# Performance work log

Hardware: AMD Instinct MI355X
Metric: run time of the kernel (lower is better)

Reference implementation:

```python
import jax, jax.numpy as jnp
import numpy as np
from jax import lax

N, S, K, V, C, D, NH, NB, HD = 4, 1024, 4, 32000, 1000, 512, 8, 6, 2048
DH = D // NH
CAP = round((S // K) * 1.0)  # expert capacity = Seq//K * capacity_factor


def setup_inputs() -> dict:
    key = jax.random.key(0)
    ks = jax.random.split(key, 12)
    nrm = lambda k, shape: jax.random.normal(k, shape, dtype=jnp.float32) * 0.02
    return dict(
        x_in=jax.random.randint(ks[0], (N, S), 0, V),
        y_target=jax.random.randint(ks[1], (N, S), 0, C),
        tok_emb=nrm(ks[2], (K, V, D)),
        pos_emb=nrm(ks[3], (K, S, D)),
        ln1_s=jnp.ones((K, NB, D)), ln1_b=jnp.zeros((K, NB, D)),
        Wqkv=nrm(ks[4], (K, NB, D, 3 * D)), bqkv=jnp.zeros((K, NB, 3 * D)),
        Wo=nrm(ks[5], (K, NB, D, D)), bo=jnp.zeros((K, NB, D)),
        ln2_s=jnp.ones((K, NB, D)), ln2_b=jnp.zeros((K, NB, D)),
        W1=nrm(ks[6], (K, NB, D, HD)), b1=jnp.zeros((K, NB, HD)),
        W2=nrm(ks[7], (K, NB, HD, D)), b2=jnp.zeros((K, NB, D)),
        lnf_s=jnp.ones((K, D)), lnf_b=jnp.zeros((K, D)),
        Wcls=nrm(ks[8], (K, D, C)), bcls=jnp.zeros((K, C)),
        Wconf=nrm(ks[9], (K, D, 1)), bconf=jnp.zeros((K, 1)),
    )


def _ln(x, s, b):
    m = x.mean(-1, keepdims=True)
    v = jnp.var(x, axis=-1, keepdims=True)
    return (x - m) * lax.rsqrt(v + 1e-5) * s + b


def reference(x_in, y_target, tok_emb, pos_emb, ln1_s, ln1_b, Wqkv, bqkv, Wo, bo,
              ln2_s, ln2_b, W1, b1, W2, b2, lnf_s, lnf_b, Wcls, bcls, Wconf, bconf):
    causal = jnp.tril(jnp.ones((S, S), dtype=bool))

    def model_fwd(te, pe, l1s, l1b, wqkv, bq, wo, bo_, l2s, l2b, w1, b1_, w2, b2_, lfs, lfb, wc, bc, wcf, bcf):
        x = te[x_in] + pe[None]  # [N,S,D]
        for i in range(NB):
            h = _ln(x, l1s[i], l1b[i])
            qkv = h @ wqkv[i] + bq[i]
            q, k, v = jnp.split(qkv, 3, axis=-1)
            q = q.reshape(N, S, NH, DH); k = k.reshape(N, S, NH, DH); v = v.reshape(N, S, NH, DH)
            att = jnp.einsum('nqhd,nkhd->nhqk', q, k) / np.float32(np.sqrt(DH))
            att = jax.nn.softmax(jnp.where(causal, att, jnp.float32(-1e9)), axis=-1)
            o = jnp.einsum('nhqk,nkhd->nqhd', att, v).reshape(N, S, D)
            x = x + o @ wo[i] + bo_[i]
            h = _ln(x, l2s[i], l2b[i])
            x = x + jax.nn.gelu(h @ w1[i] + b1_[i]) @ w2[i] + b2_[i]
        x = _ln(x, lfs, lfb)
        return x @ wc + bc, x @ wcf + bcf  # logits [N,S,C], confidence [N,S,1]

    clf, conf = jax.vmap(model_fwd)(tok_emb, pos_emb, ln1_s, ln1_b, Wqkv, bqkv, Wo, bo,
                                    ln2_s, ln2_b, W1, b1, W2, b2, lnf_s, lnf_b, Wcls, bcls, Wconf, bconf)
    combined_classifier = jnp.transpose(clf, (1, 0, 2, 3))       # [N,K,S,C]
    combined_confidence = jnp.transpose(conf[..., 0], (1, 0, 2))  # [N,K,S]

    # --- capacity-constrained auction routing on detached logits ---
    logp = jax.nn.log_softmax(lax.stop_gradient(combined_classifier), axis=-1)
    tgt = jnp.broadcast_to(y_target[:, None, :, None], (N, K, S, 1))
    loss = -jnp.take_along_axis(logp, tgt, axis=-1)[..., 0]  # per-token CE, [N,K,S]
    order = jnp.argsort(loss, axis=1, stable=True)            # [N,K,S] models sorted by loss
    order_s = jnp.transpose(order, (2, 0, 1))                 # [S,N,K]
    rows = jnp.arange(N)

    def step(tc, chunk):  # tc: token_count [N,K]; chunk: [N,K]
        tcm = jnp.take_along_axis(tc, chunk, axis=1)
        best = jnp.argmax((tcm < CAP).astype(jnp.float32), axis=1)
        chosen = chunk[rows, best]
        return tc.at[rows, chosen].add(1.0), chosen

    _, chosen = lax.scan(step, jnp.zeros((N, K), dtype=jnp.float32), order_s)
    activated_models_indices = chosen.T  # [N,S]

    mask = jax.nn.one_hot(activated_models_indices, K, dtype=combined_classifier.dtype)  # [N,S,K]
    mask = jnp.transpose(mask, (0, 2, 1))[..., None]  # [N,K,S,1]
    out = (combined_classifier * mask).sum(axis=1)    # [N,S,C]
    return out, combined_confidence, activated_models_indices
```

## Files before the change

### kernel.cpp

```cpp
#include <hip/hip_runtime.h>
#include <hip/hip_bf16.h>

#define N_  4
#define S_  1024
#define K_  4
#define V_  32000
#define C_  1000
#define D_  512
#define NH_ 8
#define NB_ 6
#define HD_ 2048
#define DH_ 64
#define CAP_ 256
#define M_  (N_*S_)

typedef __attribute__((ext_vector_type(8))) short short8_t;
typedef __attribute__((ext_vector_type(4))) float f32x4_t;

#define MFMA16(a,b,c) __builtin_amdgcn_mfma_f32_16x16x32_bf16((a),(b),(c),0,0,0)

static __device__ __forceinline__ unsigned short f2bf(float f) {
    unsigned u = __float_as_uint(f);
    unsigned r = (u + 0x7FFFu + ((u >> 16) & 1u)) >> 16;
    return (unsigned short)r;
}
static __device__ __forceinline__ float bfround(float v) {
    unsigned u = __float_as_uint(v);
    u = (u + 0x7FFFu + ((u >> 16) & 1u)) & 0xFFFF0000u;
    return __uint_as_float(u);
}
static __device__ __forceinline__ void split3(float v, unsigned short& a, unsigned short& b, unsigned short& c) {
    const float f0 = bfround(v);      const float r1 = v - f0;
    const float f1 = bfround(r1);     const float f2 = bfround(r1 - f1);
    a = (unsigned short)(__float_as_uint(f0) >> 16);
    b = (unsigned short)(__float_as_uint(f1) >> 16);
    c = (unsigned short)(__float_as_uint(f2) >> 16);
}

__global__ __launch_bounds__(256) void embed_kernel(const int* __restrict__ x_in,
    const float* __restrict__ tok, const float* __restrict__ pos, float* __restrict__ x)
{
    const int idx = blockIdx.x * 256 + threadIdx.x;
    const int total = M_ * (D_ / 4);
    if (idx >= total) return;
    const int d = (idx & (D_ / 4 - 1)) * 4;
    const int row = idx >> 7;
    const int s = row & (S_ - 1);
    const int t = x_in[row];
    const float4 a = *(const float4*)(tok + (size_t)t * D_ + d);
    const float4 b = *(const float4*)(pos + (size_t)s * D_ + d);
    float4 r; r.x = a.x + b.x; r.y = a.y + b.y; r.z = a.z + b.z; r.w = a.w + b.w;
    *(float4*)(x + (size_t)row * D_ + d) = r;
}

__global__ __launch_bounds__(256) void ln_kernel(const float* __restrict__ x,
    const float* __restrict__ sc, const float* __restrict__ bi, float* __restrict__ out)
{
    const int row = blockIdx.x, tid = threadIdx.x;
    const float* xr = x + (size_t)row * D_;
    float v0 = xr[tid], v1 = xr[tid + 256];
    float s1 = v0 + v1;
#pragma unroll
    for (int off = 32; off; off >>= 1) s1 += __shfl_down(s1, off, 64);
    __shared__ float red[8];
    __shared__ float stat[2];
    const int wid = tid >> 6, lane = tid & 63;
    if (lane == 0) red[wid] = s1;
    __syncthreads();
    if (tid == 0) stat[0] = (red[0] + red[1] + red[2] + red[3]) * (1.f / (float)D_);
    __syncthreads();
    const float mean = stat[0];
    const float d0 = v0 - mean, d1 = v1 - mean;
    float s2 = d0 * d0 + d1 * d1;
#pragma unroll
    for (int off = 32; off; off >>= 1) s2 += __shfl_down(s2, off, 64);
    if (lane == 0) red[wid] = s2;
    __syncthreads();
    if (tid == 0) stat[1] = (red[0] + red[1] + red[2] + red[3]) * (1.f / (float)D_);
    __syncthreads();
    const float rstd = rsqrtf(stat[1] + 1e-5f);
    float* orow = out + (size_t)row * D_;
    orow[tid]       = d0 * rstd * sc[tid]       + bi[tid];
    orow[tid + 256] = d1 * rstd * sc[tid + 256] + bi[tid + 256];
}

template<int EPI>
__global__ __launch_bounds__(256, 2) void sgemm_mfma(const float* __restrict__ A,
    const float* __restrict__ B, const float* __restrict__ bias, float* __restrict__ C,
    int Nc, int Kd, int lda, int ldb, int ldc)
{
    __shared__ __align__(16) unsigned short As[3][128][40];
    __shared__ __align__(16) unsigned short Bs[3][128][40];
    const int tid = threadIdx.x;
    const int bm = blockIdx.y * 128, bn = blockIdx.x * 128;
    const int wid = tid >> 6, lane = tid & 63;
    const int wm = (wid >> 1) * 64, wn = (wid & 1) * 64;
    const int lr = lane & 15, lg = lane >> 4;
    const int arow = tid >> 1, aof = (tid & 1) * 16;
    const int bcol = tid & 127, bkh = tid >> 7;
    const int gcol = bn + bcol;

    f32x4_t acc[4][4] = {};

    for (int k0 = 0; k0 < Kd; k0 += 32) {
        float afv[16], bfv[16];
        {
            const float* Ap = A + (size_t)(bm + arow) * lda + k0 + aof;
            *(float4*)&afv[0]  = ((const float4*)Ap)[0];
            *(float4*)&afv[4]  = ((const float4*)Ap)[1];
            *(float4*)&afv[8]  = ((const float4*)Ap)[2];
            *(float4*)&afv[12] = ((const float4*)Ap)[3];
        }
        if (gcol < Nc) {
            const float* Bp = B + (size_t)(k0 + bkh * 16) * ldb + gcol;
#pragma unroll
            for (int i = 0; i < 16; ++i) bfv[i] = Bp[(size_t)i * ldb];
        } else {
#pragma unroll
            for (int i = 0; i < 16; ++i) bfv[i] = 0.f;
        }
        __syncthreads();
        {
            unsigned short q0[16], q1[16], q2[16];
#pragma unroll
            for (int i = 0; i < 16; ++i) split3(afv[i], q0[i], q1[i], q2[i]);
            *(uint4*)&As[0][arow][aof] = *(uint4*)&q0[0]; *(uint4*)&As[0][arow][aof + 8] = *(uint4*)&q0[8];
            *(uint4*)&As[1][arow][aof] = *(uint4*)&q1[0]; *(uint4*)&As[1][arow][aof + 8] = *(uint4*)&q1[8];
            *(uint4*)&As[2][arow][aof] = *(uint4*)&q2[0]; *(uint4*)&As[2][arow][aof + 8] = *(uint4*)&q2[8];
        }
        {
            unsigned short q0[16], q1[16], q2[16];
#pragma unroll
            for (int i = 0; i < 16; ++i) split3(bfv[i], q0[i], q1[i], q2[i]);
            const int ko = bkh * 16;
            *(uint4*)&Bs[0][bcol][ko] = *(uint4*)&q0[0]; *(uint4*)&Bs[0][bcol][ko + 8] = *(uint4*)&q0[8];
            *(uint4*)&Bs[1][bcol][ko] = *(uint4*)&q1[0]; *(uint4*)&Bs[1][bcol][ko + 8] = *(uint4*)&q1[8];
            *(uint4*)&Bs[2][bcol][ko] = *(uint4*)&q2[0]; *(uint4*)&Bs[2][bcol][ko + 8] = *(uint4*)&q2[8];
        }
        __syncthreads();
        short8_t af[3][4], bg[3][4];
#pragma unroll
        for (int s = 0; s < 3; ++s)
#pragma unroll
            for (int m = 0; m < 4; ++m)
                af[s][m] = *(const short8_t*)&As[s][wm + m * 16 + lr][lg * 8];
#pragma unroll
        for (int s = 0; s < 3; ++s)
#pragma unroll
            for (int n = 0; n < 4; ++n)
                bg[s][n] = *(const short8_t*)&Bs[s][wn + n * 16 + lr][lg * 8];
#pragma unroll
        for (int m = 0; m < 4; ++m)
#pragma unroll
            for (int n = 0; n < 4; ++n) {
                f32x4_t c = acc[m][n];
                c = MFMA16(af[0][m], bg[0][n], c);
                c = MFMA16(af[0][m], bg[1][n], c);
                c = MFMA16(af[1][m], bg[0][n], c);
                c = MFMA16(af[1][m], bg[1][n], c);
                c = MFMA16(af[0][m], bg[2][n], c);
                c = MFMA16(af[2][m], bg[0][n], c);
                acc[m][n] = c;
            }
    }
#pragma unroll
    for (int m = 0; m < 4; ++m)
#pragma unroll
        for (int n = 0; n < 4; ++n) {
            const int col = bn + wn + n * 16 + lr;
            if (col >= Nc) continue;
            const float bv = bias ? bias[col] : 0.f;
            const int row0 = bm + wm + m * 16 + lg * 4;
#pragma unroll
            for (int r = 0; r < 4; ++r) {
                float v = acc[m][n][r] + bv;
                float* cp = C + (size_t)(row0 + r) * ldc + col;
                if (EPI == 1) v += *cp;
                if (EPI == 2) {
                    const float t = v;
                    v = 0.5f * t * (1.f + tanhf(0.7978845608028654f * (t + 0.044715f * t * t * t)));
                }
                *cp = v;
            }
        }
}

__global__ __launch_bounds__(256, 2) void cls_rerun_kernel(const unsigned short* __restrict__ A,
    const float* __restrict__ B, const float* __restrict__ bias,
    const int* __restrict__ chosen, const int kk, float* __restrict__ out)
{
    __shared__ __align__(16) unsigned short As[128][40];
    __shared__ __align__(16) unsigned short Bs[128][40];
    __shared__ int anyrow;
    const int tid = threadIdx.x;
    const int bm = blockIdx.y * 128, bn = blockIdx.x * 128;
    if (tid == 0) anyrow = 0;
    __syncthreads();
    if (tid < 128 && chosen[bm + tid] == kk) anyrow = 1;
    __syncthreads();
    if (!anyrow) return;
    const int wid = tid >> 6, lane = tid & 63;
    const int wm = (wid >> 1) * 64, wn = (wid & 1) * 64;
    const int lr = lane & 15, lg = lane >> 4;
    const int arow = tid >> 1, aof = (tid & 1) * 16;
    const int bcol = tid & 127, bkh = tid >> 7;
    const int gcol = bn + bcol;

    f32x4_t acc[4][4] = {};
    for (int k0 = 0; k0 < D_; k0 += 32) {
        const unsigned short* Ap = A + (size_t)(bm + arow) * D_ + k0 + aof;
        const uint4 av0 = ((const uint4*)Ap)[0];
        const uint4 av1 = ((const uint4*)Ap)[1];
        float bfv[16];
        if (gcol < C_) {
            const float* Bp = B + (size_t)(k0 + bkh * 16) * C_ + gcol;
#pragma unroll
            for (int i = 0; i < 16; ++i) bfv[i] = Bp[(size_t)i * C_];
        } else {
#pragma unroll
            for (int i = 0; i < 16; ++i) bfv[i] = 0.f;
        }
        __syncthreads();
        *(uint4*)&As[arow][aof] = av0;
        *(uint4*)&As[arow][aof + 8] = av1;
        {
            unsigned short q0[16];
#pragma unroll
            for (int i = 0; i < 16; ++i) q0[i] = f2bf(bfv[i]);
            const int ko = bkh * 16;
            *(uint4*)&Bs[bcol][ko] = *(uint4*)&q0[0];
            *(uint4*)&Bs[bcol][ko + 8] = *(uint4*)&q0[8];
        }
        __syncthreads();
        short8_t af[4], bg[4];
#pragma unroll
        for (int m = 0; m < 4; ++m) af[m] = *(const short8_t*)&As[wm + m * 16 + lr][lg * 8];
#pragma unroll
        for (int n = 0; n < 4; ++n) bg[n] = *(const short8_t*)&Bs[wn + n * 16 + lr][lg * 8];
#pragma unroll
        for (int m = 0; m < 4; ++m)
#pragma unroll
            for (int n = 0; n < 4; ++n)
                acc[m][n] = MFMA16(af[m], bg[n], acc[m][n]);
    }
#pragma unroll
    for (int m = 0; m < 4; ++m)
#pragma unroll
        for (int n = 0; n < 4; ++n) {
            const int col = bn + wn + n * 16 + lr;
            if (col >= C_) continue;
            const float bv = bias[col];
            const int row0 = bm + wm + m * 16 + lg * 4;
#pragma unroll
            for (int r = 0; r < 4; ++r) {
                const int row = row0 + r;
                if (chosen[row] == kk) out[(size_t)row * C_ + col] = acc[m][n][r] + bv;
            }
        }
}

__global__ __launch_bounds__(256) void attn_mfma_kernel(const float* __restrict__ qkv, float* __restrict__ O)
{
    __shared__ __align__(16) unsigned short Ks[3][32][72];
    __shared__ __align__(16) unsigned short Vt[3][64][40];
    __shared__ __align__(16) unsigned short Ps[4][3][16][40];
    const int qt = blockIdx.x, hh = blockIdx.y, n = blockIdx.z;
    const int tid = threadIdx.x;
    const int w = tid >> 6, lane = tid & 63;
    const int lr = lane & 15, lg = lane >> 4;
    const size_t rs = 3 * D_;
    const float* base = qkv + (size_t)n * S_ * rs + hh * DH_;

    short8_t qf[3][2];
    {
        const int qrow = qt * 64 + w * 16 + lr;
#pragma unroll
        for (int ks = 0; ks < 2; ++ks) {
            const float* qp = base + (size_t)qrow * rs + ks * 32 + lg * 8;
            float v[8];
            *(float4*)&v[0] = ((const float4*)qp)[0];
            *(float4*)&v[4] = ((const float4*)qp)[1];
#pragma unroll
            for (int j = 0; j < 8; ++j) {
                unsigned short a, b, c;
                split3(v[j], a, b, c);
                qf[0][ks][j] = (short)a; qf[1][ks][j] = (short)b; qf[2][ks][j] = (short)c;
            }
        }
    }

    f32x4_t oacc[4] = {};
    float m_r[4], l_r[4];
#pragma unroll
    for (int r = 0; r < 4; ++r) { m_r[r] = -1e30f; l_r[r] = 0.f; }

    const int ktmax = 2 * qt + 2;
    for (int kt = 0; kt < ktmax; ++kt) {
        __syncthreads();
        {
            const int key = tid & 31, seg = tid >> 5;
            const float* kp = base + (size_t)(kt * 32 + key) * rs + D_ + seg * 8;
            const float* vp = kp + D_;
            float kv[8], vv[8];
            *(float4*)&kv[0] = ((const float4*)kp)[0];
            *(float4*)&kv[4] = ((const float4*)kp)[1];
            *(float4*)&vv[0] = ((const float4*)vp)[0];
            *(float4*)&vv[4] = ((const float4*)vp)[1];
            unsigned short k0a[8], k1a[8], k2a[8];
#pragma unroll
            for (int j = 0; j < 8; ++j) split3(kv[j], k0a[j], k1a[j], k2a[j]);
            *(uint4*)&Ks[0][key][seg * 8] = *(uint4*)&k0a[0];
            *(uint4*)&Ks[1][key][seg * 8] = *(uint4*)&k1a[0];
            *(uint4*)&Ks[2][key][seg * 8] = *(uint4*)&k2a[0];
#pragma unroll
            for (int j = 0; j < 8; ++j) {
                unsigned short a, b, c;
                split3(vv[j], a, b, c);
                Vt[0][seg * 8 + j][key] = a;
                Vt[1][seg * 8 + j][key] = b;
                Vt[2][seg * 8 + j][key] = c;
            }
        }
        __syncthreads();
        f32x4_t sacc[2] = {};
#pragma unroll
        for (int n2 = 0; n2 < 2; ++n2) {
#pragma unroll
            for (int ks = 0; ks < 2; ++ks) {
                short8_t kb0 = *(const short8_t*)&Ks[0][n2 * 16 + lr][ks * 32 + lg * 8];
                short8_t kb1 = *(const short8_t*)&Ks[1][n2 * 16 + lr][ks * 32 + lg * 8];
                short8_t kb2 = *(const short8_t*)&Ks[2][n2 * 16 + lr][ks * 32 + lg * 8];
                f32x4_t c = sacc[n2];
                c = MFMA16(qf[0][ks], kb0, c);
                c = MFMA16(qf[0][ks], kb1, c);
                c = MFMA16(qf[1][ks], kb0, c);
                c = MFMA16(qf[1][ks], kb1, c);
                c = MFMA16(qf[0][ks], kb2, c);
                c = MFMA16(qf[2][ks], kb0, c);
                sacc[n2] = c;
            }
        }
        float p[2][4];
#pragma unroll
        for (int n2 = 0; n2 < 2; ++n2)
#pragma unroll
            for (int r = 0; r < 4; ++r) {
                float s = sacc[n2][r] * 0.125f;
                const int key = kt * 32 + n2 * 16 + lr;
                const int qrow = qt * 64 + w * 16 + lg * 4 + r;
                if (key > qrow) s = -1e30f;
                p[n2][r] = s;
            }
        float scl[4];
#pragma unroll
        for (int r = 0; r < 4; ++r) {
            float tm = fmaxf(p[0][r], p[1][r]);
            tm = fmaxf(tm, __shfl_xor(tm, 1));
            tm = fmaxf(tm, __shfl_xor(tm, 2));
            tm = fmaxf(tm, __shfl_xor(tm, 4));
            tm = fmaxf(tm, __shfl_xor(tm, 8));
            const float mnew = fmaxf(m_r[r], tm);
            scl[r] = expf(m_r[r] - mnew);
            m_r[r] = mnew;
        }
#pragma unroll
        for (int r = 0; r < 4; ++r) {
            p[0][r] = expf(p[0][r] - m_r[r]);
            p[1][r] = expf(p[1][r] - m_r[r]);
            float ts = p[0][r] + p[1][r];
            ts += __shfl_xor(ts, 1);
            ts += __shfl_xor(ts, 2);
            ts += __shfl_xor(ts, 4);
            ts += __shfl_xor(ts, 8);
            l_r[r] = l_r[r] * scl[r] + ts;
        }
#pragma unroll
        for (int nf = 0; nf < 4; ++nf)
#pragma unroll
            for (int r = 0; r < 4; ++r) oacc[nf][r] *= scl[r];
#pragma unroll
        for (int n2 = 0; n2 < 2; ++n2)
#pragma unroll
            for (int r = 0; r < 4; ++r) {
                unsigned short a, b, c;
                split3(p[n2][r], a, b, c);
                Ps[w][0][lg * 4 + r][n2 * 16 + lr] = a;
                Ps[w][1][lg * 4 + r][n2 * 16 + lr] = b;
                Ps[w][2][lg * 4 + r][n2 * 16 + lr] = c;
            }
        short8_t pa0 = *(const short8_t*)&Ps[w][0][lr][lg * 8];
        short8_t pa1 = *(const short8_t*)&Ps[w][1][lr][lg * 8];
        short8_t pa2 = *(const short8_t*)&Ps[w][2][lr][lg * 8];
#pragma unroll
        for (int nf = 0; nf < 4; ++nf) {
            short8_t vb0 = *(const short8_t*)&Vt[0][nf * 16 + lr][lg * 8];
            short8_t vb1 = *(const short8_t*)&Vt[1][nf * 16 + lr][lg * 8];
            short8_t vb2 = *(const short8_t*)&Vt[2][nf * 16 + lr][lg * 8];
            f32x4_t c = oacc[nf];
            c = MFMA16(pa0, vb0, c);
            c = MFMA16(pa0, vb1, c);
            c = MFMA16(pa1, vb0, c);
            c = MFMA16(pa1, vb1, c);
            c = MFMA16(pa0, vb2, c);
            c = MFMA16(pa2, vb0, c);
            oacc[nf] = c;
        }
    }
    float inv[4];
#pragma unroll
    for (int r = 0; r < 4; ++r) inv[r] = 1.f / l_r[r];
#pragma unroll
    for (int nf = 0; nf < 4; ++nf)
#pragma unroll
        for (int r = 0; r < 4; ++r) {
            const int qrow = qt * 64 + w * 16 + lg * 4 + r;
            O[((size_t)n * S_ + qrow) * D_ + hh * DH_ + nf * 16 + lr] = oacc[nf][r] * inv[r];
        }
}

__global__ __launch_bounds__(256) void cast_kernel(const float* __restrict__ src,
    unsigned short* __restrict__ dst)
{
    const int idx = blockIdx.x * 256 + threadIdx.x;
    const int total = M_ * D_ / 4;
    if (idx >= total) return;
    const float4 v = ((const float4*)src)[idx];
    ushort4 o;
    o.x = f2bf(v.x); o.y = f2bf(v.y); o.z = f2bf(v.z); o.w = f2bf(v.w);
    ((ushort4*)dst)[idx] = o;
}

__global__ __launch_bounds__(256) void conf_kernel(const float* __restrict__ h,
    const float* __restrict__ w, const float* __restrict__ bc, float* __restrict__ conf_out, int k)
{
    const int wid = threadIdx.x >> 6, lane = threadIdx.x & 63;
    const int row = blockIdx.x * 4 + wid;
    const float* hr = h + (size_t)row * D_;
    float sm = 0.f;
#pragma unroll
    for (int j = 0; j < 8; ++j) sm += hr[lane + 64 * j] * w[lane + 64 * j];
#pragma unroll
    for (int off = 32; off; off >>= 1) sm += __shfl_down(sm, off, 64);
    if (lane == 0) {
        const int n = row >> 10, s = row & (S_ - 1);
        conf_out[((size_t)n * K_ + k) * S_ + s] = sm + bc[0];
    }
}

__global__ __launch_bounds__(256) void loss_kernel(const float* __restrict__ logits,
    const int* __restrict__ y, float* __restrict__ loss)
{
    const int row = blockIdx.x;
    const float* lr = logits + (size_t)row * C_;
    const int tid = threadIdx.x;
    __shared__ float red[256];
    float mx = -1e30f;
    for (int c = tid; c < C_; c += 256) mx = fmaxf(mx, lr[c]);
    red[tid] = mx; __syncthreads();
    for (int st = 128; st > 0; st >>= 1) {
        if (tid < st) red[tid] = fmaxf(red[tid], red[tid + st]);
        __syncthreads();
    }
    mx = red[0];
    __syncthreads();
    float sm = 0.f;
    for (int c = tid; c < C_; c += 256) sm += expf(lr[c] - mx);
    red[tid] = sm; __syncthreads();
    for (int st = 128; st > 0; st >>= 1) {
        if (tid < st) red[tid] += red[tid + st];
        __syncthreads();
    }
    if (tid == 0) loss[row] = logf(red[0]) + mx - lr[y[row]];
}

__global__ __launch_bounds__(256) void routing_kernel(const float* __restrict__ loss,
    float* __restrict__ idx_out, int* __restrict__ chosen_buf)
{
    __shared__ float l_s[K_][S_];
    __shared__ unsigned char ord_s[S_];
    const int n = blockIdx.x;
    const int tid = threadIdx.x;
#pragma unroll
    for (int k = 0; k < K_; ++k)
        ((float4*)l_s[k])[tid] = ((const float4*)(loss + (size_t)k * M_ + n * S_))[tid];
    __syncthreads();
    for (int s = tid; s < S_; s += 256) {
        float l[K_];
#pragma unroll
        for (int k = 0; k < K_; ++k) l[k] = l_s[k][s];
        int ord[K_] = {0, 1, 2, 3};
#pragma unroll
        for (int i = 1; i < K_; ++i) {
            const int v = ord[i];
            int j = i;
            while (j > 0 && l[ord[j - 1]] > l[v]) { ord[j] = ord[j - 1]; --j; }
            ord[j] = v;
        }
        ord_s[s] = (unsigned char)(ord[0] | (ord[1] << 2) | (ord[2] << 4) | (ord[3] << 6));
    }
    __syncthreads();
    if (tid == 0) {
        int tc[K_] = {0, 0, 0, 0};
        for (int s = 0; s < S_; ++s) {
            const unsigned b = ord_s[s];
            int ch = b & 3;
#pragma unroll
            for (int j = 0; j < K_; ++j) {
                const int m = (b >> (2 * j)) & 3;
                if (tc[m] < CAP_) { ch = m; break; }
            }
            ++tc[ch];
            chosen_buf[n * S_ + s] = ch;
            idx_out[n * S_ + s] = (float)ch;
        }
    }
}

extern "C" void kernel_launch(void* const* d_in, const int* in_sizes, int n_in,
                              void* d_out, int out_size, void* d_ws, size_t ws_size,
                              hipStream_t stream)
{
    const int*   x_in = (const int*)d_in[0];
    const int*   y    = (const int*)d_in[1];
    const float* tok  = (const float*)d_in[2];
    const float* pos  = (const float*)d_in[3];
    const float* ln1s = (const float*)d_in[4];
    const float* ln1b = (const float*)d_in[5];
    const float* Wqkv = (const float*)d_in[6];
    const float* bqkv = (const float*)d_in[7];
    const float* Wo   = (const float*)d_in[8];
    const float* bo   = (const float*)d_in[9];
    const float* ln2s = (const float*)d_in[10];
    const float* ln2b = (const float*)d_in[11];
    const float* W1   = (const float*)d_in[12];
    const float* b1   = (const float*)d_in[13];
    const float* W2   = (const float*)d_in[14];
    const float* b2   = (const float*)d_in[15];
    const float* lnfs = (const float*)d_in[16];
    const float* lnfb = (const float*)d_in[17];
    const float* Wcls = (const float*)d_in[18];
    const float* bcls = (const float*)d_in[19];
    const float* Wcnf = (const float*)d_in[20];
    const float* bcnf = (const float*)d_in[21];

    float* R = (float*)d_ws;
    unsigned short* hfin = (unsigned short*)(R + (size_t)M_ * 3 * D_);
    float* x    = (float*)(hfin + (size_t)K_ * M_ * D_);
    float* h    = x + (size_t)M_ * D_;
    float* loss = h + (size_t)M_ * D_;
    int*   chosen = (int*)(loss + (size_t)K_ * M_);

    float* out      = (float*)d_out;
    float* conf_out = out + (size_t)M_ * C_;
    float* idx_out  = conf_out + (size_t)N_ * K_ * S_;

    for (int k = 0; k < K_; ++k) {
        embed_kernel<<<(M_ * (D_ / 4) + 255) / 256, 256, 0, stream>>>(
            x_in, tok + (size_t)k * V_ * D_, pos + (size_t)k * S_ * D_, x);
        for (int i = 0; i < NB_; ++i) {
            const size_t ki = (size_t)k * NB_ + i;
            ln_kernel<<<M_, 256, 0, stream>>>(x, ln1s + ki * D_, ln1b + ki * D_, h);
            sgemm_mfma<0><<<dim3(12, 32), 256, 0, stream>>>(
                h, Wqkv + ki * D_ * 3 * D_, bqkv + ki * 3 * D_, R, 3 * D_, D_, D_, 3 * D_, 3 * D_);
            attn_mfma_kernel<<<dim3(S_ / 64, NH_, N_), 256, 0, stream>>>(R, h);
            sgemm_mfma<1><<<dim3(4, 32), 256, 0, stream>>>(
                h, Wo + ki * D_ * D_, bo + ki * D_, x, D_, D_, D_, D_, D_);
            ln_kernel<<<M_, 256, 0, stream>>>(x, ln2s + ki * D_, ln2b + ki * D_, h);
            for (int c = 0; c < 2; ++c) {
                sgemm_mfma<2><<<dim3(8, 32), 256, 0, stream>>>(
                    h, W1 + ki * D_ * HD_ + c * 1024, b1 + ki * HD_ + c * 1024, R,
                    1024, D_, D_, HD_, 1024);
                sgemm_mfma<1><<<dim3(4, 32), 256, 0, stream>>>(
                    R, W2 + ki * HD_ * D_ + (size_t)c * 1024 * D_, (c == 0) ? (b2 + ki * D_) : nullptr,
                    x, D_, 1024, 1024, D_, D_);
            }
        }
        ln_kernel<<<M_, 256, 0, stream>>>(x, lnfs + (size_t)k * D_, lnfb + (size_t)k * D_, h);
        cast_kernel<<<(M_ * D_ / 4 + 255) / 256, 256, 0, stream>>>(h, hfin + (size_t)k * M_ * D_);
        sgemm_mfma<0><<<dim3(8, 32), 256, 0, stream>>>(
            h, Wcls + (size_t)k * D_ * C_, bcls + (size_t)k * C_, R, C_, D_, D_, C_, C_);
        conf_kernel<<<M_ / 4, 256, 0, stream>>>(h, Wcnf + (size_t)k * D_, bcnf + k, conf_out, k);
        loss_kernel<<<M_, 256, 0, stream>>>(R, y, loss + (size_t)k * M_);
    }
    routing_kernel<<<N_, 256, 0, stream>>>(loss, idx_out, chosen);
    for (int k = 0; k < K_; ++k)
        cls_rerun_kernel<<<dim3(8, 32), 256, 0, stream>>>(
            hfin + (size_t)k * M_ * D_, Wcls + (size_t)k * D_ * C_, bcls + (size_t)k * C_,
            chosen, k, out);
}
```

Measured before the change: 14.51 ms.

## Pre-split activations and weights into bf16 planes outside the GEMM main loop

```diff
diff --git a/kernel.cpp b/kernel.cpp
--- a/kernel.cpp
+++ b/kernel.cpp
@@ -19,11 +19,9 @@
 
 #define MFMA16(a,b,c) __builtin_amdgcn_mfma_f32_16x16x32_bf16((a),(b),(c),0,0,0)
 
-static __device__ __forceinline__ unsigned short f2bf(float f) {
-    unsigned u = __float_as_uint(f);
-    unsigned r = (u + 0x7FFFu + ((u >> 16) & 1u)) >> 16;
-    return (unsigned short)r;
-}
+#define HSPLANE ((size_t)M_ * D_)
+#define WTMAX   ((size_t)524288)
+
 static __device__ __forceinline__ float bfround(float v) {
     unsigned u = __float_as_uint(v);
     u = (u + 0x7FFFu + ((u >> 16) & 1u)) & 0xFFFF0000u;
@@ -35,6 +33,9 @@
     a = (unsigned short)(__float_as_uint(f0) >> 16);
     b = (unsigned short)(__float_as_uint(f1) >> 16);
     c = (unsigned short)(__float_as_uint(f2) >> 16);
+}
+static __device__ __forceinline__ float b2f(unsigned short u) {
+    return __uint_as_float((unsigned)u << 16);
 }
 
 __global__ __launch_bounds__(256) void embed_kernel(const int* __restrict__ x_in,
@@ -54,7 +55,7 @@
 }
 
 __global__ __launch_bounds__(256) void ln_kernel(const float* __restrict__ x,
-    const float* __restrict__ sc, const float* __restrict__ bi, float* __restrict__ out)
+    const float* __restrict__ sc, const float* __restrict__ bi, unsigned short* __restrict__ hs)
 {
     const int row = blockIdx.x, tid = threadIdx.x;
     const float* xr = x + (size_t)row * D_;
@@ -79,187 +80,163 @@
     if (tid == 0) stat[1] = (red[0] + red[1] + red[2] + red[3]) * (1.f / (float)D_);
     __syncthreads();
     const float rstd = rsqrtf(stat[1] + 1e-5f);
-    float* orow = out + (size_t)row * D_;
-    orow[tid]       = d0 * rstd * sc[tid]       + bi[tid];
-    orow[tid + 256] = d1 * rstd * sc[tid + 256] + bi[tid + 256];
+    const float o0 = d0 * rstd * sc[tid] + bi[tid];
+    const float o1 = d1 * rstd * sc[tid + 256] + bi[tid + 256];
+    unsigned short a, b, c;
+    const size_t base = (size_t)row * D_ + tid;
+    split3(o0, a, b, c);
+    hs[base] = a; hs[base + HSPLANE] = b; hs[base + 2 * HSPLANE] = c;
+    split3(o1, a, b, c);
+    hs[base + 256] = a; hs[base + 256 + HSPLANE] = b; hs[base + 256 + 2 * HSPLANE] = c;
+}
+
+__global__ __launch_bounds__(256) void wsplit_kernel(const float* __restrict__ W, int ldw, int NcTrue,
+    unsigned short* __restrict__ Wt, size_t bplane, int Kd)
+{
+    const int tid = threadIdx.x;
+    const int n = blockIdx.x * 64 + (tid & 63);
+    const int k0 = blockIdx.y * 32 + (tid >> 6) * 8;
+    unsigned short q0[8], q1[8], q2[8];
+    if (n < NcTrue) {
+#pragma unroll
+        for (int j = 0; j < 8; ++j) split3(W[(size_t)(k0 + j) * ldw + n], q0[j], q1[j], q2[j]);
+    } else {
+#pragma unroll
+        for (int j = 0; j < 8; ++j) { q0[j] = 0; q1[j] = 0; q2[j] = 0; }
+    }
+    unsigned short* dst = Wt + (size_t)n * Kd + k0;
+    *(uint4*)dst = *(uint4*)&q0[0];
+    *(uint4*)(dst + bplane) = *(uint4*)&q1[0];
+    *(uint4*)(dst + 2 * bplane) = *(uint4*)&q2[0];
 }
 
 template<int EPI>
-__global__ __launch_bounds__(256, 2) void sgemm_mfma(const float* __restrict__ A,
-    const float* __restrict__ B, const float* __restrict__ bias, float* __restrict__ C,
-    int Nc, int Kd, int lda, int ldb, int ldc)
-{
-    __shared__ __align__(16) unsigned short As[3][128][40];
-    __shared__ __align__(16) unsigned short Bs[3][128][40];
+__global__ __launch_bounds__(256) void gemm64(const unsigned short* __restrict__ A3, size_t aplane,
+    const unsigned short* __restrict__ Bt, size_t bplane, const float* __restrict__ bias,
+    void* __restrict__ Cv, size_t cplane, int Nc, int Kd, int lda, int ldc)
+{
+    __shared__ __align__(16) unsigned short Bs[3][64][40];
     const int tid = threadIdx.x;
-    const int bm = blockIdx.y * 128, bn = blockIdx.x * 128;
+    const int bm = blockIdx.y * 128, bn = blockIdx.x * 64;
     const int wid = tid >> 6, lane = tid & 63;
-    const int wm = (wid >> 1) * 64, wn = (wid & 1) * 64;
+    const int wm = (wid >> 1) * 64, wn = (wid & 1) * 32;
     const int lr = lane & 15, lg = lane >> 4;
-    const int arow = tid >> 1, aof = (tid & 1) * 16;
-    const int bcol = tid & 127, bkh = tid >> 7;
-    const int gcol = bn + bcol;
-
-    f32x4_t acc[4][4] = {};
+    const int scol = tid >> 2, skq = tid & 3;
+    const unsigned short* Bp0 = Bt + (size_t)(bn + scol) * Kd + skq * 8;
+
+    f32x4_t acc[4][2] = {};
 
     for (int k0 = 0; k0 < Kd; k0 += 32) {
-        float afv[16], bfv[16];
-        {
-            const float* Ap = A + (size_t)(bm + arow) * lda + k0 + aof;
-            *(float4*)&afv[0]  = ((const float4*)Ap)[0];
-            *(float4*)&afv[4]  = ((const float4*)Ap)[1];
-            *(float4*)&afv[8]  = ((const float4*)Ap)[2];
-            *(float4*)&afv[12] = ((const float4*)Ap)[3];
-        }
-        if (gcol < Nc) {
-            const float* Bp = B + (size_t)(k0 + bkh * 16) * ldb + gcol;
-#pragma unroll
-            for (int i = 0; i < 16; ++i) bfv[i] = Bp[(size_t)i * ldb];
-        } else {
-#pragma unroll
-            for (int i = 0; i < 16; ++i) bfv[i] = 0.f;
+        const uint4 bq0 = *(const uint4*)(Bp0 + k0);
+        const uint4 bq1 = *(const uint4*)(Bp0 + bplane + k0);
+        const uint4 bq2 = *(const uint4*)(Bp0 + 2 * bplane + k0);
+        short8_t af[3][4];
+#pragma unroll
+        for (int m = 0; m < 4; ++m) {
+            const unsigned short* ap = A3 + (size_t)(bm + wm + m * 16 + lr) * lda + k0 + lg * 8;
+            af[0][m] = *(const short8_t*)ap;
+            af[1][m] = *(const short8_t*)(ap + aplane);
+            af[2][m] = *(const short8_t*)(ap + 2 * aplane);
         }
         __syncthreads();
-        {
-            unsigned short q0[16], q1[16], q2[16];
-#pragma unroll
-            for (int i = 0; i < 16; ++i) split3(afv[i], q0[i], q1[i], q2[i]);
-            *(uint4*)&As[0][arow][aof] = *(uint4*)&q0[0]; *(uint4*)&As[0][arow][aof + 8] = *(uint4*)&q0[8];
-            *(uint4*)&As[1][arow][aof] = *(uint4*)&q1[0]; *(uint4*)&As[1][arow][aof + 8] = *(uint4*)&q1[8];
-            *(uint4*)&As[2][arow][aof] = *(uint4*)&q2[0]; *(uint4*)&As[2][arow][aof + 8] = *(uint4*)&q2[8];
-        }
-        {
-            unsigned short q0[16], q1[16], q2[16];
-#pragma unroll
-            for (int i = 0; i < 16; ++i) split3(bfv[i], q0[i], q1[i], q2[i]);
-            const int ko = bkh * 16;
-            *(uint4*)&Bs[0][bcol][ko] = *(uint4*)&q0[0]; *(uint4*)&Bs[0][bcol][ko + 8] = *(uint4*)&q0[8];
-            *(uint4*)&Bs[1][bcol][ko] = *(uint4*)&q1[0]; *(uint4*)&Bs[1][bcol][ko + 8] = *(uint4*)&q1[8];
-            *(uint4*)&Bs[2][bcol][ko] = *(uint4*)&q2[0]; *(uint4*)&Bs[2][bcol][ko + 8] = *(uint4*)&q2[8];
-        }
+        *(uint4*)&Bs[0][scol][skq * 8] = bq0;
+        *(uint4*)&Bs[1][scol][skq * 8] = bq1;
+        *(uint4*)&Bs[2][scol][skq * 8] = bq2;
         __syncthreads();
-        short8_t af[3][4], bg[3][4];
+        short8_t bg[3][2];
 #pragma unroll
         for (int s = 0; s < 3; ++s)
 #pragma unroll
-            for (int m = 0; m < 4; ++m)
-                af[s][m] = *(const short8_t*)&As[s][wm + m * 16 + lr][lg * 8];
-#pragma unroll
-        for (int s = 0; s < 3; ++s)
-#pragma unroll
-            for (int n = 0; n < 4; ++n)
-                bg[s][n] = *(const short8_t*)&Bs[s][wn + n * 16 + lr][lg * 8];
+            for (int n2 = 0; n2 < 2; ++n2)
+                bg[s][n2] = *(const short8_t*)&Bs[s][wn + n2 * 16 + lr][lg * 8];
 #pragma unroll
         for (int m = 0; m < 4; ++m)
 #pragma unroll
-            for (int n = 0; n < 4; ++n) {
-                f32x4_t c = acc[m][n];
-                c = MFMA16(af[0][m], bg[0][n], c);
-                c = MFMA16(af[0][m], bg[1][n], c);
-                c = MFMA16(af[1][m], bg[0][n], c);
-                c = MFMA16(af[1][m], bg[1][n], c);
-                c = MFMA16(af[0][m], bg[2][n], c);
-                c = MFMA16(af[2][m], bg[0][n], c);
-                acc[m][n] = c;
+            for (int n2 = 0; n2 < 2; ++n2) {
+                f32x4_t c = acc[m][n2];
+                c = MFMA16(af[0][m], bg[0][n2], c);
+                c = MFMA16(af[0][m], bg[1][n2], c);
+                c = MFMA16(af[1][m], bg[0][n2], c);
+                c = MFMA16(af[1][m], bg[1][n2], c);
+                c = MFMA16(af[0][m], bg[2][n2], c);
+                c = MFMA16(af[2][m], bg[0][n2], c);
+                acc[m][n2] = c;
             }
     }
 #pragma unroll
     for (int m = 0; m < 4; ++m)
 #pragma unroll
-        for (int n = 0; n < 4; ++n) {
-            const int col = bn + wn + n * 16 + lr;
+        for (int n2 = 0; n2 < 2; ++n2) {
+            const int col = bn + wn + n2 * 16 + lr;
             if (col >= Nc) continue;
             const float bv = bias ? bias[col] : 0.f;
             const int row0 = bm + wm + m * 16 + lg * 4;
 #pragma unroll
             for (int r = 0; r < 4; ++r) {
-                float v = acc[m][n][r] + bv;
-                float* cp = C + (size_t)(row0 + r) * ldc + col;
-                if (EPI == 1) v += *cp;
+                float v = acc[m][n2][r] + bv;
                 if (EPI == 2) {
                     const float t = v;
-                    v = 0.5f * t * (1.f + tanhf(0.7978845608028654f * (t + 0.044715f * t * t * t)));
+                    const float g = 0.5f * t * (1.f + tanhf(0.7978845608028654f * (t + 0.044715f * t * t * t)));
+                    unsigned short a, b, c;
+                    split3(g, a, b, c);
+                    unsigned short* Cp = (unsigned short*)Cv + (size_t)(row0 + r) * ldc + col;
+                    Cp[0] = a; Cp[cplane] = b; Cp[2 * cplane] = c;
+                } else {
+                    float* cp = (float*)Cv + (size_t)(row0 + r) * ldc + col;
+                    if (EPI == 1) v += *cp;
+                    *cp = v;
                 }
-                *cp = v;
-            }
-        }
-}
-
-__global__ __launch_bounds__(256, 2) void cls_rerun_kernel(const unsigned short* __restrict__ A,
-    const float* __restrict__ B, const float* __restrict__ bias,
+            }
+        }
+}
+
+__global__ __launch_bounds__(256) void rerun_kernel(const unsigned short* __restrict__ A,
+    const unsigned short* __restrict__ B0, const float* __restrict__ bias,
     const int* __restrict__ chosen, const int kk, float* __restrict__ out)
 {
-    __shared__ __align__(16) unsigned short As[128][40];
-    __shared__ __align__(16) unsigned short Bs[128][40];
     __shared__ int anyrow;
     const int tid = threadIdx.x;
-    const int bm = blockIdx.y * 128, bn = blockIdx.x * 128;
+    const int bm = blockIdx.y * 128, bn = blockIdx.x * 64;
     if (tid == 0) anyrow = 0;
     __syncthreads();
     if (tid < 128 && chosen[bm + tid] == kk) anyrow = 1;
     __syncthreads();
     if (!anyrow) return;
     const int wid = tid >> 6, lane = tid & 63;
-    const int wm = (wid >> 1) * 64, wn = (wid & 1) * 64;
+    const int wm = (wid >> 1) * 64, wn = (wid & 1) * 32;
     const int lr = lane & 15, lg = lane >> 4;
-    const int arow = tid >> 1, aof = (tid & 1) * 16;
-    const int bcol = tid & 127, bkh = tid >> 7;
-    const int gcol = bn + bcol;
-
-    f32x4_t acc[4][4] = {};
+    f32x4_t acc[4][2] = {};
     for (int k0 = 0; k0 < D_; k0 += 32) {
-        const unsigned short* Ap = A + (size_t)(bm + arow) * D_ + k0 + aof;
-        const uint4 av0 = ((const uint4*)Ap)[0];
-        const uint4 av1 = ((const uint4*)Ap)[1];
-        float bfv[16];
-        if (gcol < C_) {
-            const float* Bp = B + (size_t)(k0 + bkh * 16) * C_ + gcol;
-#pragma unroll
-            for (int i = 0; i < 16; ++i) bfv[i] = Bp[(size_t)i * C_];
-        } else {
-#pragma unroll
-            for (int i = 0; i < 16; ++i) bfv[i] = 0.f;
-        }
-        __syncthreads();
-        *(uint4*)&As[arow][aof] = av0;
-        *(uint4*)&As[arow][aof + 8] = av1;
-        {
-            unsigned short q0[16];
-#pragma unroll
-            for (int i = 0; i < 16; ++i) q0[i] = f2bf(bfv[i]);
-            const int ko = bkh * 16;
-            *(uint4*)&Bs[bcol][ko] = *(uint4*)&q0[0];
-            *(uint4*)&Bs[bcol][ko + 8] = *(uint4*)&q0[8];
-        }
-        __syncthreads();
-        short8_t af[4], bg[4];
-#pragma unroll
-        for (int m = 0; m < 4; ++m) af[m] = *(const short8_t*)&As[wm + m * 16 + lr][lg * 8];
-#pragma unroll
-        for (int n = 0; n < 4; ++n) bg[n] = *(const short8_t*)&Bs[wn + n * 16 + lr][lg * 8];
+        short8_t af[4], bg[2];
 #pragma unroll
         for (int m = 0; m < 4; ++m)
-#pragma unroll
-            for (int n = 0; n < 4; ++n)
-                acc[m][n] = MFMA16(af[m], bg[n], acc[m][n]);
+            af[m] = *(const short8_t*)(A + (size_t)(bm + wm + m * 16 + lr) * D_ + k0 + lg * 8);
+#pragma unroll
+        for (int n2 = 0; n2 < 2; ++n2)
+            bg[n2] = *(const short8_t*)(B0 + (size_t)(bn + wn + n2 * 16 + lr) * D_ + k0 + lg * 8);
+#pragma unroll
+        for (int m = 0; m < 4; ++m)
+#pragma unroll
+            for (int n2 = 0; n2 < 2; ++n2)
+                acc[m][n2] = MFMA16(af[m], bg[n2], acc[m][n2]);
     }
 #pragma unroll
     for (int m = 0; m < 4; ++m)
 #pragma unroll
-        for (int n = 0; n < 4; ++n) {
-            const int col = bn + wn + n * 16 + lr;
+        for (int n2 = 0; n2 < 2; ++n2) {
+            const int col = bn + wn + n2 * 16 + lr;
             if (col >= C_) continue;
             const float bv = bias[col];
             const int row0 = bm + wm + m * 16 + lg * 4;
 #pragma unroll
             for (int r = 0; r < 4; ++r) {
                 const int row = row0 + r;
-                if (chosen[row] == kk) out[(size_t)row * C_ + col] = acc[m][n][r] + bv;
-            }
-        }
-}
-
-__global__ __launch_bounds__(256) void attn_mfma_kernel(const float* __restrict__ qkv, float* __restrict__ O)
+                if (chosen[row] == kk) out[(size_t)row * C_ + col] = acc[m][n2][r] + bv;
+            }
+        }
+}
+
+__global__ __launch_bounds__(256) void attn_mfma_kernel(const float* __restrict__ qkv, unsigned short* __restrict__ hsO)
 {
     __shared__ __align__(16) unsigned short Ks[3][32][72];
     __shared__ __align__(16) unsigned short Vt[3][64][40];
@@ -414,31 +391,26 @@
 #pragma unroll
         for (int r = 0; r < 4; ++r) {
             const int qrow = qt * 64 + w * 16 + lg * 4 + r;
-            O[((size_t)n * S_ + qrow) * D_ + hh * DH_ + nf * 16 + lr] = oacc[nf][r] * inv[r];
-        }
-}
-
-__global__ __launch_bounds__(256) void cast_kernel(const float* __restrict__ src,
-    unsigned short* __restrict__ dst)
-{
-    const int idx = blockIdx.x * 256 + threadIdx.x;
-    const int total = M_ * D_ / 4;
-    if (idx >= total) return;
-    const float4 v = ((const float4*)src)[idx];
-    ushort4 o;
-    o.x = f2bf(v.x); o.y = f2bf(v.y); o.z = f2bf(v.z); o.w = f2bf(v.w);
-    ((ushort4*)dst)[idx] = o;
-}
-
-__global__ __launch_bounds__(256) void conf_kernel(const float* __restrict__ h,
+            const size_t idx = ((size_t)n * S_ + qrow) * D_ + hh * DH_ + nf * 16 + lr;
+            unsigned short a, b, c;
+            split3(oacc[nf][r] * inv[r], a, b, c);
+            hsO[idx] = a; hsO[idx + HSPLANE] = b; hsO[idx + 2 * HSPLANE] = c;
+        }
+}
+
+__global__ __launch_bounds__(256) void conf_kernel(const unsigned short* __restrict__ hs,
     const float* __restrict__ w, const float* __restrict__ bc, float* __restrict__ conf_out, int k)
 {
     const int wid = threadIdx.x >> 6, lane = threadIdx.x & 63;
     const int row = blockIdx.x * 4 + wid;
-    const float* hr = h + (size_t)row * D_;
+    const unsigned short* h0 = hs + (size_t)row * D_;
+    const unsigned short* h1 = h0 + HSPLANE;
     float sm = 0.f;
 #pragma unroll
-    for (int j = 0; j < 8; ++j) sm += hr[lane + 64 * j] * w[lane + 64 * j];
+    for (int j = 0; j < 8; ++j) {
+        const int i = lane + 64 * j;
+        sm += (b2f(h0[i]) + b2f(h1[i])) * w[i];
+    }
 #pragma unroll
     for (int off = 32; off; off >>= 1) sm += __shfl_down(sm, off, 64);
     if (lane == 0) {
@@ -543,12 +515,16 @@
     const float* Wcnf = (const float*)d_in[20];
     const float* bcnf = (const float*)d_in[21];
 
+    if (ws_size < 66142208) return;
     float* R = (float*)d_ws;
-    unsigned short* hfin = (unsigned short*)(R + (size_t)M_ * 3 * D_);
-    float* x    = (float*)(hfin + (size_t)K_ * M_ * D_);
-    float* h    = x + (size_t)M_ * D_;
-    float* loss = h + (size_t)M_ * D_;
-    int*   chosen = (int*)(loss + (size_t)K_ * M_);
+    unsigned short* hs   = (unsigned short*)(R + (size_t)M_ * 1536);
+    float* x             = (float*)(hs + 3 * HSPLANE);
+    unsigned short* hfin = (unsigned short*)(x + (size_t)M_ * D_);
+    unsigned short* Wt   = hfin + (size_t)K_ * M_ * D_;
+    float* loss          = (float*)(Wt + 3 * WTMAX);
+    int*   chosen        = (int*)(loss + (size_t)K_ * M_);
+    unsigned short* mids = (unsigned short*)R;
+    const size_t midplane = (size_t)M_ * 1024;
 
     float* out      = (float*)d_out;
     float* conf_out = out + (size_t)M_ * C_;
@@ -559,32 +535,47 @@
             x_in, tok + (size_t)k * V_ * D_, pos + (size_t)k * S_ * D_, x);
         for (int i = 0; i < NB_; ++i) {
             const size_t ki = (size_t)k * NB_ + i;
-            ln_kernel<<<M_, 256, 0, stream>>>(x, ln1s + ki * D_, ln1b + ki * D_, h);
-            sgemm_mfma<0><<<dim3(12, 32), 256, 0, stream>>>(
-                h, Wqkv + ki * D_ * 3 * D_, bqkv + ki * 3 * D_, R, 3 * D_, D_, D_, 3 * D_, 3 * D_);
-            attn_mfma_kernel<<<dim3(S_ / 64, NH_, N_), 256, 0, stream>>>(R, h);
-            sgemm_mfma<1><<<dim3(4, 32), 256, 0, stream>>>(
-                h, Wo + ki * D_ * D_, bo + ki * D_, x, D_, D_, D_, D_, D_);
-            ln_kernel<<<M_, 256, 0, stream>>>(x, ln2s + ki * D_, ln2b + ki * D_, h);
+            ln_kernel<<<M_, 256, 0, stream>>>(x, ln1s + ki * D_, ln1b + ki * D_, hs);
             for (int c = 0; c < 2; ++c) {
-                sgemm_mfma<2><<<dim3(8, 32), 256, 0, stream>>>(
-                    h, W1 + ki * D_ * HD_ + c * 1024, b1 + ki * HD_ + c * 1024, R,
-                    1024, D_, D_, HD_, 1024);
-                sgemm_mfma<1><<<dim3(4, 32), 256, 0, stream>>>(
-                    R, W2 + ki * HD_ * D_ + (size_t)c * 1024 * D_, (c == 0) ? (b2 + ki * D_) : nullptr,
-                    x, D_, 1024, 1024, D_, D_);
-            }
-        }
-        ln_kernel<<<M_, 256, 0, stream>>>(x, lnfs + (size_t)k * D_, lnfb + (size_t)k * D_, h);
-        cast_kernel<<<(M_ * D_ / 4 + 255) / 256, 256, 0, stream>>>(h, hfin + (size_t)k * M_ * D_);
-        sgemm_mfma<0><<<dim3(8, 32), 256, 0, stream>>>(
-            h, Wcls + (size_t)k * D_ * C_, bcls + (size_t)k * C_, R, C_, D_, D_, C_, C_);
-        conf_kernel<<<M_ / 4, 256, 0, stream>>>(h, Wcnf + (size_t)k * D_, bcnf + k, conf_out, k);
+                wsplit_kernel<<<dim3(12, 16), 256, 0, stream>>>(
+                    Wqkv + ki * D_ * 3 * D_ + c * 768, 3 * D_, 768, Wt, 768 * 512, D_);
+                gemm64<0><<<dim3(12, 32), 256, 0, stream>>>(
+                    hs, HSPLANE, Wt, 768 * 512, bqkv + ki * 3 * D_ + c * 768,
+                    R + c * 768, 0, 768, D_, D_, 3 * D_);
+            }
+            attn_mfma_kernel<<<dim3(S_ / 64, NH_, N_), 256, 0, stream>>>(R, hs);
+            wsplit_kernel<<<dim3(8, 16), 256, 0, stream>>>(Wo + ki * D_ * D_, D_, D_, Wt, 512 * 512, D_);
+            gemm64<1><<<dim3(8, 32), 256, 0, stream>>>(
+                hs, HSPLANE, Wt, 512 * 512, bo + ki * D_, x, 0, D_, D_, D_, D_);
+            ln_kernel<<<M_, 256, 0, stream>>>(x, ln2s + ki * D_, ln2b + ki * D_, hs);
+            for (int c = 0; c < 2; ++c) {
+                wsplit_kernel<<<dim3(16, 16), 256, 0, stream>>>(
+                    W1 + ki * D_ * HD_ + c * 1024, HD_, 1024, Wt, 1024 * 512, D_);
+                gemm64<2><<<dim3(16, 32), 256, 0, stream>>>(
+                    hs, HSPLANE, Wt, 1024 * 512, b1 + ki * HD_ + c * 1024,
+                    mids, midplane, 1024, D_, D_, 1024);
+                wsplit_kernel<<<dim3(8, 32), 256, 0, stream>>>(
+                    W2 + ki * HD_ * D_ + (size_t)c * 1024 * D_, D_, D_, Wt, 512 * 1024, 1024);
+                gemm64<1><<<dim3(8, 32), 256, 0, stream>>>(
+                    mids, midplane, Wt, 512 * 1024, (c == 0) ? (b2 + ki * D_) : nullptr,
+                    x, 0, D_, 1024, 1024, D_);
+            }
+        }
+        ln_kernel<<<M_, 256, 0, stream>>>(x, lnfs + (size_t)k * D_, lnfb + (size_t)k * D_, hs);
+        hipMemcpyAsync(hfin + (size_t)k * M_ * D_, hs, (size_t)M_ * D_ * 2,
+                       hipMemcpyDeviceToDevice, stream);
+        wsplit_kernel<<<dim3(16, 16), 256, 0, stream>>>(
+            Wcls + (size_t)k * D_ * C_, C_, C_, Wt, 1024 * 512, D_);
+        gemm64<0><<<dim3(16, 32), 256, 0, stream>>>(
+            hs, HSPLANE, Wt, 1024 * 512, bcls + (size_t)k * C_, R, 0, C_, D_, D_, C_);
+        conf_kernel<<<M_ / 4, 256, 0, stream>>>(hs, Wcnf + (size_t)k * D_, bcnf + k, conf_out, k);
         loss_kernel<<<M_, 256, 0, stream>>>(R, y, loss + (size_t)k * M_);
     }
     routing_kernel<<<N_, 256, 0, stream>>>(loss, idx_out, chosen);
-    for (int k = 0; k < K_; ++k)
-        cls_rerun_kernel<<<dim3(8, 32), 256, 0, stream>>>(
-            hfin + (size_t)k * M_ * D_, Wcls + (size_t)k * D_ * C_, bcls + (size_t)k * C_,
-            chosen, k, out);
-}
+    for (int k = 0; k < K_; ++k) {
+        wsplit_kernel<<<dim3(16, 16), 256, 0, stream>>>(
+            Wcls + (size_t)k * D_ * C_, C_, C_, Wt, 1024 * 512, D_);
+        rerun_kernel<<<dim3(16, 32), 256, 0, stream>>>(
+            hfin + (size_t)k * M_ * D_, Wt, bcls + (size_t)k * C_, chosen, k, out);
+    }
+}
```

Result: faster. 13.85 ms (-4.6%).
